# Performance work log

Hardware: AMD Instinct MI355X
Metric: run time of the kernel (lower is better)

Reference implementation:

```python
import jax, jax.numpy as jnp
import numpy as np

K = 7          # kernel_size
PAD = 3        # (K + (K-1)*(dilation-1) - 1)//2 with dilation=1
G = 16         # groups = channels // group_channels = 256 // 16
GC = 16        # group_channels (hardcoded in module)
BN_EPS = 1e-5


def setup_inputs() -> dict:
    key = jax.random.key(0)
    ks = jax.random.split(key, 6)
    C = 256
    Cr = C // 4           # 64
    O2 = K * K * G        # 784
    x = jax.random.normal(ks[0], (4, C, 56, 56), dtype=jnp.float32)
    w1 = jax.random.normal(ks[1], (Cr, C), dtype=jnp.float32) * (1.0 / np.sqrt(C))
    bn_gamma = jnp.ones((Cr,), dtype=jnp.float32)
    bn_beta = jnp.zeros((Cr,), dtype=jnp.float32)
    bn_mean = jax.random.normal(ks[2], (Cr,), dtype=jnp.float32) * 0.1
    bn_var = jax.random.uniform(ks[3], (Cr,), dtype=jnp.float32, minval=0.5, maxval=1.5)
    w2 = jax.random.normal(ks[4], (O2, Cr), dtype=jnp.float32) * (1.0 / np.sqrt(Cr))
    b2 = jnp.zeros((O2,), dtype=jnp.float32)
    return {"x": x, "w1": w1, "bn_gamma": bn_gamma, "bn_beta": bn_beta,
            "bn_mean": bn_mean, "bn_var": bn_var, "w2": w2, "b2": b2}


def reference(x, w1, bn_gamma, bn_beta, bn_mean, bn_var, w2, b2):
    b, C, H, W = x.shape
    # --- weight branch: conv1 (1x1) + BN(eval) + ReLU, then conv2 (1x1) ---
    y = jnp.einsum('oc,bchw->bohw', w1, x)
    scale = bn_gamma * jax.lax.rsqrt(bn_var + BN_EPS)
    y = jax.nn.relu(y * scale[None, :, None, None]
                    + (bn_beta - bn_mean * scale)[None, :, None, None])
    w = jnp.einsum('oc,bchw->bohw', w2, y) + b2[None, :, None, None]
    w = w.reshape(b, G, K * K, H, W)                       # per-pixel dynamic kernels
    # --- unfold: overlapping KxK patches (stride=1, dilation=1, pad=3) ---
    xp = jnp.pad(x, ((0, 0), (0, 0), (PAD, PAD), (PAD, PAD)))
    patches = jnp.stack([xp[:, :, i:i + H, j:j + W]
                         for i in range(K) for j in range(K)], axis=2)  # [b,C,K2,H,W]
    patches = patches.reshape(b, G, GC, K * K, H, W)
    # --- dynamic multiply-reduce over kernel positions ---
    out = jnp.einsum('bgkhw,bgckhw->bgchw', w, patches)
    return out.reshape(b, C, H, W)
```

## Files before the change

kernel.cpp:

```cpp
#include <hip/hip_runtime.h>


#define HW    3136
#define WIDE  56
#define C_IN  256
#define CR    64
#define GC    16
#define KK    49
#define BN_EPS 1e-5f

typedef __attribute__((ext_vector_type(8))) short short8;
typedef __attribute__((ext_vector_type(4))) float f32x4;
typedef __attribute__((ext_vector_type(2))) unsigned int u32x2;

__device__ __forceinline__ unsigned short f2bf(float f) {
    unsigned u = __float_as_uint(f);
    return (unsigned short)((u + 0x7FFFu + ((u >> 16) & 1u)) >> 16);
}

__global__ __launch_bounds__(256) void prep_kernel(
    const float* __restrict__ w1, const float* __restrict__ w2,
    const float* __restrict__ b2,
    unsigned short* __restrict__ w1bf, unsigned short* __restrict__ wprep,
    float* __restrict__ b2pad)
{
    const int t = blockIdx.x * 256 + threadIdx.x;
    if (t < 16384) {
        w1bf[t] = f2bf(w1[t]);
    }
    {
        const int g = t >> 12, k = (t >> 6) & 63, c = t & 63;
        wprep[t] = (k < KK) ? f2bf(w2[(size_t)(g * KK + k) * CR + c]) : (unsigned short)0;
    }
    if (t < 1024) {
        const int g = t >> 6, k = t & 63;
        b2pad[t] = (k < KK) ? b2[g * KK + k] : 0.f;
    }
}

__device__ __forceinline__ int xs_byte(int px, int c) {
    return ((px << 9) + (c << 1)) ^ ((px & 7) << 4);
}

__global__ __launch_bounds__(256) void conv1_bn_relu(
    const float* __restrict__ x, const unsigned short* __restrict__ w1bf,
    const float* __restrict__ gamma, const float* __restrict__ beta,
    const float* __restrict__ mean, const float* __restrict__ var,
    unsigned short* __restrict__ ybf)
{
    __shared__ unsigned short xs[64 * 256];

    const int t    = threadIdx.x;
    const int lane = t & 63;
    const int q    = __builtin_amdgcn_readfirstlane(t >> 6);
    const int tile = blockIdx.x;
    const int b    = tile / 49;
    const int hw0  = (tile - b * 49) * 64;

    {
        const int px = lane;
        const int cb = q * 64;
        const float* __restrict__ xb = x + ((size_t)b * C_IN + cb) * HW + hw0 + px;
#pragma unroll
        for (int i = 0; i < 8; ++i) {
            short8 pk;
#pragma unroll
            for (int j = 0; j < 8; ++j)
                pk[j] = (short)f2bf(xb[(size_t)(i * 8 + j) * HW]);
            *(short8*)((char*)xs + xs_byte(px, cb + i * 8)) = pk;
        }
    }
    __syncthreads();

    const int l15 = lane & 15;
    const int lg  = lane >> 4;
    const int px  = q * 16 + l15;

    f32x4 acc[4];
#pragma unroll
    for (int mt = 0; mt < 4; ++mt) acc[mt] = (f32x4){0.f, 0.f, 0.f, 0.f};

#pragma unroll
    for (int kk = 0; kk < 8; ++kk) {
        const short8 Bf = *(const short8*)((const char*)xs + xs_byte(px, kk * 32 + lg * 8));
#pragma unroll
        for (int mt = 0; mt < 4; ++mt) {
            const short8 Af = *(const short8*)(w1bf + (mt * 16 + l15) * C_IN + kk * 32 + lg * 8);
            acc[mt] = __builtin_amdgcn_mfma_f32_16x16x32_bf16(Af, Bf, acc[mt], 0, 0, 0);
        }
    }

#pragma unroll
    for (int mt = 0; mt < 4; ++mt) {
        const int o0 = mt * 16 + lg * 4;
        const f32x4 ga = *(const f32x4*)(gamma + o0);
        const f32x4 be = *(const f32x4*)(beta + o0);
        const f32x4 mn = *(const f32x4*)(mean + o0);
        const f32x4 va = *(const f32x4*)(var + o0);
        unsigned short o4[4];
#pragma unroll
        for (int r = 0; r < 4; ++r) {
            const float sc = ga[r] * rsqrtf(va[r] + BN_EPS);
            const float sh = be[r] - mn[r] * sc;
            o4[r] = f2bf(fmaxf(acc[mt][r] * sc + sh, 0.f));
        }
        u32x2 pk;
        pk.x = (unsigned)o4[0] | ((unsigned)o4[1] << 16);
        pk.y = (unsigned)o4[2] | ((unsigned)o4[3] << 16);
        *(u32x2*)(ybf + ((size_t)(b * HW + hw0 + px)) * 64 + o0) = pk;
    }
}

__global__ __launch_bounds__(64) void conv2_involution(
    const float* __restrict__ x, const unsigned short* __restrict__ ybf,
    const unsigned short* __restrict__ wprep, const float* __restrict__ b2pad,
    float* __restrict__ out)
{
    __shared__ float kw_lds[64 * 64];

    const int tid  = threadIdx.x;
    const int l15  = tid & 15;
    const int lg   = tid >> 4;
    const int tile = blockIdx.x;
    const int g    = blockIdx.y & 15;
    const int b    = blockIdx.y >> 4;

    {
        short8 Bf[4][2], Af[4][2];
#pragma unroll
        for (int ct = 0; ct < 4; ++ct) {
            const int hwp = tile * 64 + ct * 16 + l15;
            const unsigned short* yb = ybf + ((size_t)(b * HW + hwp)) * 64 + lg * 8;
            Bf[ct][0] = *(const short8*)(yb);
            Bf[ct][1] = *(const short8*)(yb + 32);
        }
#pragma unroll
        for (int rt = 0; rt < 4; ++rt) {
            const unsigned short* ar = wprep + g * 4096 + (rt * 16 + l15) * 64 + lg * 8;
            Af[rt][0] = *(const short8*)(ar);
            Af[rt][1] = *(const short8*)(ar + 32);
        }
        f32x4 acc[4][4];
#pragma unroll
        for (int ct = 0; ct < 4; ++ct)
#pragma unroll
            for (int rt = 0; rt < 4; ++rt) {
                acc[ct][rt] = (f32x4){0.f, 0.f, 0.f, 0.f};
                acc[ct][rt] = __builtin_amdgcn_mfma_f32_16x16x32_bf16(Af[rt][0], Bf[ct][0], acc[ct][rt], 0, 0, 0);
                acc[ct][rt] = __builtin_amdgcn_mfma_f32_16x16x32_bf16(Af[rt][1], Bf[ct][1], acc[ct][rt], 0, 0, 0);
            }

        float bias[4][4];
#pragma unroll
        for (int rt = 0; rt < 4; ++rt)
#pragma unroll
            for (int r = 0; r < 4; ++r)
                bias[rt][r] = b2pad[g * 64 + rt * 16 + lg * 4 + r];

#pragma unroll
        for (int ct = 0; ct < 4; ++ct) {
            const int pxc = ct * 16 + l15;
            const int hwp = tile * 64 + pxc;
            const int hp  = hwp / WIDE;
            const int wp  = hwp - hp * WIDE;
#pragma unroll
            for (int rt = 0; rt < 4; ++rt)
#pragma unroll
                for (int r = 0; r < 4; ++r) {
                    const int k  = rt * 16 + lg * 4 + r;
                    const int i7 = k / 7, j7 = k - i7 * 7;
                    const int rr = hp + i7 - 3, cc = wp + j7 - 3;
                    const bool valid = (k < KK) & (rr >= 0) & (rr < WIDE) &
                                       (cc >= 0) & (cc < WIDE);
                    kw_lds[k * 64 + pxc] = valid ? (acc[ct][rt][r] + bias[rt][r]) : 0.f;
                }
        }
    }
    __syncthreads();

    const int pg   = tid & 15;
    const int cq   = tid >> 4;
    const int hw4  = tile * 64 + pg * 4;
    const int hrow = hw4 / WIDE;
    const int hcol = hw4 - hrow * WIDE;

    const float* bp[4];
#pragma unroll
    for (int c = 0; c < 4; ++c)
        bp[c] = x + ((size_t)b * C_IN + g * GC + cq * 4 + c) * HW;

    float acc2[4][4];
#pragma unroll
    for (int c = 0; c < 4; ++c)
#pragma unroll
        for (int p = 0; p < 4; ++p) acc2[c][p] = 0.f;

#pragma unroll
    for (int i = 0; i < 7; ++i) {
        const int rc    = min(max(hrow + i - 3, 0), WIDE - 1);
        const int basef = rc * WIDE + hcol;
        const int i0 = max(basef - 4, 0);
        const int i2 = min(basef + 4, HW - 4);

        float win[4][12];
#pragma unroll
        for (int c = 0; c < 4; ++c) {
            const f32x4 A0 = *(const f32x4*)(bp[c] + i0);
            const f32x4 A1 = *(const f32x4*)(bp[c] + basef);
            const f32x4 A2 = *(const f32x4*)(bp[c] + i2);
#pragma unroll
            for (int e = 0; e < 4; ++e) {
                win[c][e]     = A0[e];
                win[c][e + 4] = A1[e];
                win[c][e + 8] = A2[e];
            }
        }
#pragma unroll
        for (int jj = 0; jj < 7; ++jj) {
            const f32x4 kw4 = *(const f32x4*)&kw_lds[(i * 7 + jj) * 64 + pg * 4];
#pragma unroll
            for (int c = 0; c < 4; ++c)
#pragma unroll
                for (int p = 0; p < 4; ++p)
                    acc2[c][p] += kw4[p] * win[c][p + jj + 1];
        }
    }

#pragma unroll
    for (int c = 0; c < 4; ++c) {
        f32x4 st;
#pragma unroll
        for (int p = 0; p < 4; ++p) st[p] = acc2[c][p];
        *(f32x4*)(out + ((size_t)b * C_IN + g * GC + cq * 4 + c) * HW + hw4) = st;
    }
}

extern "C" void kernel_launch(void* const* d_in, const int* in_sizes, int n_in,
                              void* d_out, int out_size, void* d_ws, size_t ws_size,
                              hipStream_t stream) {
    const float* x     = (const float*)d_in[0];
    const float* w1    = (const float*)d_in[1];
    const float* gamma = (const float*)d_in[2];
    const float* beta  = (const float*)d_in[3];
    const float* mean  = (const float*)d_in[4];
    const float* var   = (const float*)d_in[5];
    const float* w2    = (const float*)d_in[6];
    const float* b2    = (const float*)d_in[7];
    float* out = (float*)d_out;

    char* ws = (char*)d_ws;
    unsigned short* ybf   = (unsigned short*)(ws);
    unsigned short* wprep = (unsigned short*)(ws + 1605632);
    float*          b2pad = (float*)(ws + 1736704);
    unsigned short* w1bf  = (unsigned short*)(ws + 1740800);

    prep_kernel<<<dim3(256), dim3(256), 0, stream>>>(w1, w2, b2, w1bf, wprep, b2pad);
    conv1_bn_relu<<<dim3(196), dim3(256), 0, stream>>>(x, w1bf, gamma, beta, mean, var, ybf);
    conv2_involution<<<dim3(49, 64), dim3(64), 0, stream>>>(x, ybf, wprep, b2pad, out);
}
```

Baseline: 40.85 us.

## Stage input halo rows in LDS and double threads per involution block

The involution kernel now cooperatively loads a 9-row halo of the 16 group channels into shared memory, with zero-padded column borders. The 7x7 window is then read from LDS instead of from global memory with clamped indices. The block grows to 128 threads (two waves), and each thread now handles 2 channels instead of 4. The MFMA weight generation is split across the two waves, each doing two column tiles. This cuts redundant global loads and raises parallelism, at the cost of more LDS use (about 51KB) and possible bank conflicts, which may limit occupancy.

```diff
diff --git a/kernel.cpp b/kernel.cpp
--- a/kernel.cpp
+++ b/kernel.cpp
@@ -111,69 +111,86 @@
     }
 }
 
-__global__ __launch_bounds__(64) void conv2_involution(
+__global__ __launch_bounds__(128) void conv2_involution(
     const float* __restrict__ x, const unsigned short* __restrict__ ybf,
     const unsigned short* __restrict__ wprep, const float* __restrict__ b2pad,
     float* __restrict__ out)
 {
-    __shared__ float kw_lds[64 * 64];
+    __shared__ float xs[16 * 612];
+    __shared__ float kw_lds[KK * 64];
 
     const int tid  = threadIdx.x;
-    const int l15  = tid & 15;
-    const int lg   = tid >> 4;
     const int tile = blockIdx.x;
     const int g    = blockIdx.y & 15;
     const int b    = blockIdx.y >> 4;
-
-    {
-        short8 Bf[4][2], Af[4][2];
-#pragma unroll
-        for (int ct = 0; ct < 4; ++ct) {
-            const int hwp = tile * 64 + ct * 16 + l15;
+    const int r0   = (tile * 64) / WIDE;
+    const int base_row = r0 - 3;
+
+    {
+        const float* __restrict__ xg = x + ((size_t)b * C_IN + g * GC) * HW;
+#pragma unroll
+        for (int it = 0; it < 16; ++it) {
+            const int id = it * 128 + tid;
+            if (id < 2016) {
+                const int c   = id / 126;
+                const int rem = id - c * 126;
+                const int j   = rem / 14;
+                const int c4  = rem - j * 14;
+                const int gr  = min(max(base_row + j, 0), WIDE - 1);
+                const f32x4 v = *(const f32x4*)(xg + (size_t)c * HW + gr * WIDE + c4 * 4);
+                *(f32x4*)&xs[c * 612 + j * 68 + 4 + c4 * 4] = v;
+            }
+        }
+#pragma unroll
+        for (int it = 0; it < 3; ++it) {
+            const int p = it * 128 + tid;
+            if (p < 288) {
+                const int c    = p / 18;
+                const int rem  = p - c * 18;
+                const int j    = rem >> 1;
+                const int side = rem & 1;
+                *(f32x4*)&xs[c * 612 + j * 68 + (side ? 60 : 0)] = (f32x4){0.f, 0.f, 0.f, 0.f};
+            }
+        }
+    }
+
+    {
+        const int lane = tid & 63;
+        const int wv   = __builtin_amdgcn_readfirstlane(tid >> 6);
+        const int l15  = lane & 15;
+        const int lg   = lane >> 4;
+#pragma unroll
+        for (int cti = 0; cti < 2; ++cti) {
+            const int ct  = wv + cti * 2;
+            const int px  = ct * 16 + l15;
+            const int hwp = tile * 64 + px;
             const unsigned short* yb = ybf + ((size_t)(b * HW + hwp)) * 64 + lg * 8;
-            Bf[ct][0] = *(const short8*)(yb);
-            Bf[ct][1] = *(const short8*)(yb + 32);
-        }
-#pragma unroll
-        for (int rt = 0; rt < 4; ++rt) {
-            const unsigned short* ar = wprep + g * 4096 + (rt * 16 + l15) * 64 + lg * 8;
-            Af[rt][0] = *(const short8*)(ar);
-            Af[rt][1] = *(const short8*)(ar + 32);
-        }
-        f32x4 acc[4][4];
-#pragma unroll
-        for (int ct = 0; ct < 4; ++ct)
+            const short8 B0 = *(const short8*)(yb);
+            const short8 B1 = *(const short8*)(yb + 32);
+            const int hp = hwp / WIDE;
+            const int wp = hwp - hp * WIDE;
+
 #pragma unroll
             for (int rt = 0; rt < 4; ++rt) {
-                acc[ct][rt] = (f32x4){0.f, 0.f, 0.f, 0.f};
-                acc[ct][rt] = __builtin_amdgcn_mfma_f32_16x16x32_bf16(Af[rt][0], Bf[ct][0], acc[ct][rt], 0, 0, 0);
-                acc[ct][rt] = __builtin_amdgcn_mfma_f32_16x16x32_bf16(Af[rt][1], Bf[ct][1], acc[ct][rt], 0, 0, 0);
-            }
-
-        float bias[4][4];
-#pragma unroll
-        for (int rt = 0; rt < 4; ++rt)
-#pragma unroll
-            for (int r = 0; r < 4; ++r)
-                bias[rt][r] = b2pad[g * 64 + rt * 16 + lg * 4 + r];
-
-#pragma unroll
-        for (int ct = 0; ct < 4; ++ct) {
-            const int pxc = ct * 16 + l15;
-            const int hwp = tile * 64 + pxc;
-            const int hp  = hwp / WIDE;
-            const int wp  = hwp - hp * WIDE;
-#pragma unroll
-            for (int rt = 0; rt < 4; ++rt)
+                const unsigned short* ar = wprep + g * 4096 + (rt * 16 + l15) * 64 + lg * 8;
+                const short8 A0 = *(const short8*)(ar);
+                const short8 A1 = *(const short8*)(ar + 32);
+                f32x4 acc = (f32x4){0.f, 0.f, 0.f, 0.f};
+                acc = __builtin_amdgcn_mfma_f32_16x16x32_bf16(A0, B0, acc, 0, 0, 0);
+                acc = __builtin_amdgcn_mfma_f32_16x16x32_bf16(A1, B1, acc, 0, 0, 0);
 #pragma unroll
                 for (int r = 0; r < 4; ++r) {
-                    const int k  = rt * 16 + lg * 4 + r;
-                    const int i7 = k / 7, j7 = k - i7 * 7;
-                    const int rr = hp + i7 - 3, cc = wp + j7 - 3;
-                    const bool valid = (k < KK) & (rr >= 0) & (rr < WIDE) &
-                                       (cc >= 0) & (cc < WIDE);
-                    kw_lds[k * 64 + pxc] = valid ? (acc[ct][rt][r] + bias[rt][r]) : 0.f;
+                    const int k = rt * 16 + lg * 4 + r;
+                    if (k < KK) {
+                        const float val = acc[r] + b2pad[g * 64 + k];
+                        const int i7 = k / 7, j7 = k - i7 * 7;
+                        const int rr = hp + i7 - 3, cc = wp + j7 - 3;
+                        const bool valid = (rr >= 0) & (rr < WIDE) &
+                                           (cc >= 0) & (cc < WIDE);
+                        kw_lds[k * 64 + px] = valid ? val : 0.f;
+                    }
                 }
+            }
         }
     }
     __syncthreads();
@@ -183,56 +200,56 @@
     const int hw4  = tile * 64 + pg * 4;
     const int hrow = hw4 / WIDE;
     const int hcol = hw4 - hrow * WIDE;
-
-    const float* bp[4];
-#pragma unroll
-    for (int c = 0; c < 4; ++c)
-        bp[c] = x + ((size_t)b * C_IN + g * GC + cq * 4 + c) * HW;
-
-    float acc2[4][4];
-#pragma unroll
-    for (int c = 0; c < 4; ++c)
+    const int srow = hrow - r0;
+
+    const int xb0 = (cq * 2) * 612 + srow * 68 + hcol;
+
+    float acc2[2][4];
+#pragma unroll
+    for (int c = 0; c < 2; ++c)
 #pragma unroll
         for (int p = 0; p < 4; ++p) acc2[c][p] = 0.f;
 
 #pragma unroll
     for (int i = 0; i < 7; ++i) {
-        const int rc    = min(max(hrow + i - 3, 0), WIDE - 1);
-        const int basef = rc * WIDE + hcol;
-        const int i0 = max(basef - 4, 0);
-        const int i2 = min(basef + 4, HW - 4);
-
-        float win[4][12];
-#pragma unroll
-        for (int c = 0; c < 4; ++c) {
-            const f32x4 A0 = *(const f32x4*)(bp[c] + i0);
-            const f32x4 A1 = *(const f32x4*)(bp[c] + basef);
-            const f32x4 A2 = *(const f32x4*)(bp[c] + i2);
+        const int rb0 = xb0 + i * 68;
+        const int rb1 = rb0 + 612;
+
+        float win[2][12];
+        {
+            const f32x4 A0 = *(const f32x4*)&xs[rb0];
+            const f32x4 A1 = *(const f32x4*)&xs[rb0 + 4];
+            const f32x4 A2 = *(const f32x4*)&xs[rb0 + 8];
+            const f32x4 B0 = *(const f32x4*)&xs[rb1];
+            const f32x4 B1 = *(const f32x4*)&xs[rb1 + 4];
+            const f32x4 B2 = *(const f32x4*)&xs[rb1 + 8];
 #pragma unroll
             for (int e = 0; e < 4; ++e) {
-                win[c][e]     = A0[e];
-                win[c][e + 4] = A1[e];
-                win[c][e + 8] = A2[e];
+                win[0][e]     = A0[e];
+                win[0][e + 4] = A1[e];
+                win[0][e + 8] = A2[e];
+                win[1][e]     = B0[e];
+                win[1][e + 4] = B1[e];
+                win[1][e + 8] = B2[e];
             }
         }
 #pragma unroll
         for (int jj = 0; jj < 7; ++jj) {
             const f32x4 kw4 = *(const f32x4*)&kw_lds[(i * 7 + jj) * 64 + pg * 4];
 #pragma unroll
-            for (int c = 0; c < 4; ++c)
+            for (int c = 0; c < 2; ++c)
 #pragma unroll
                 for (int p = 0; p < 4; ++p)
                     acc2[c][p] += kw4[p] * win[c][p + jj + 1];
         }
     }
 
-#pragma unroll
-    for (int c = 0; c < 4; ++c) {
-        f32x4 st;
-#pragma unroll
-        for (int p = 0; p < 4; ++p) st[p] = acc2[c][p];
-        *(f32x4*)(out + ((size_t)b * C_IN + g * GC + cq * 4 + c) * HW + hw4) = st;
-    }
+    f32x4 st0, st1;
+#pragma unroll
+    for (int p = 0; p < 4; ++p) { st0[p] = acc2[0][p]; st1[p] = acc2[1][p]; }
+    float* __restrict__ ob = out + ((size_t)b * C_IN + g * GC + cq * 2) * HW + hw4;
+    *(f32x4*)(ob)      = st0;
+    *(f32x4*)(ob + HW) = st1;
 }
 
 extern "C" void kernel_launch(void* const* d_in, const int* in_sizes, int n_in,
@@ -256,5 +273,5 @@
 
     prep_kernel<<<dim3(256), dim3(256), 0, stream>>>(w1, w2, b2, w1bf, wprep, b2pad);
     conv1_bn_relu<<<dim3(196), dim3(256), 0, stream>>>(x, w1bf, gamma, beta, mean, var, ybf);
-    conv2_involution<<<dim3(49, 64), dim3(64), 0, stream>>>(x, ybf, wprep, b2pad, out);
-}
+    conv2_involution<<<dim3(49, 64), dim3(128), 0, stream>>>(x, ybf, wprep, b2pad, out);
+}
```

Measured after the change: 64.03 us. 56.8% more time.

## Stage x as zero-padded bf16 planes for involution window loads

Applied to the files above, without the earlier changes.

Adds a pre-pass kernel that converts x to bf16 and stores each channel plane with a 3-pixel zero border (62x64 rows). The involution stage then reads its 7x7 windows from this padded bf16 buffer, which removes the per-row clamp and index arithmetic and halves the bytes fetched per window. The cost is an extra kernel launch and an extra full pass over x, and rounding the patch values to bf16 loses some precision compared with the fp32 reads.

```diff
diff --git a/kernel.cpp b/kernel.cpp
--- a/kernel.cpp
+++ b/kernel.cpp
@@ -8,14 +8,21 @@
 #define GC    16
 #define KK    49
 #define BN_EPS 1e-5f
+#define PROW  62
+#define PCOL  64
+#define PSTR  (PROW * PCOL)
 
 typedef __attribute__((ext_vector_type(8))) short short8;
+typedef __attribute__((ext_vector_type(4))) short s16x4;
 typedef __attribute__((ext_vector_type(4))) float f32x4;
 typedef __attribute__((ext_vector_type(2))) unsigned int u32x2;
 
 __device__ __forceinline__ unsigned short f2bf(float f) {
     unsigned u = __float_as_uint(f);
     return (unsigned short)((u + 0x7FFFu + ((u >> 16) & 1u)) >> 16);
+}
+__device__ __forceinline__ float bf2f(unsigned short v) {
+    return __uint_as_float(((unsigned)v) << 16);
 }
 
 __global__ __launch_bounds__(256) void prep_kernel(
@@ -36,6 +43,37 @@
         const int g = t >> 6, k = t & 63;
         b2pad[t] = (k < KK) ? b2[g * KK + k] : 0.f;
     }
+}
+
+__global__ __launch_bounds__(256) void xpad_kernel(
+    const float* __restrict__ x, unsigned short* __restrict__ xbf)
+{
+    const int id = blockIdx.x * 256 + threadIdx.x;
+    if (id >= 1024 * PROW) return;
+    const int plane = id / PROW;
+    const int prow  = id - plane * PROW;
+    const int gr    = prow - 3;
+
+    unsigned short row[PCOL];
+    if (gr >= 0 && gr < WIDE) {
+        const float* __restrict__ src = x + (size_t)plane * HW + gr * WIDE;
+#pragma unroll
+        for (int e = 0; e < 4; ++e) { row[e] = 0; row[60 + e] = 0; }
+#pragma unroll
+        for (int v = 0; v < 14; ++v) {
+            const f32x4 a = *(const f32x4*)(src + v * 4);
+#pragma unroll
+            for (int e = 0; e < 4; ++e) row[4 + v * 4 + e] = f2bf(a[e]);
+        }
+    } else {
+#pragma unroll
+        for (int e = 0; e < PCOL; ++e) row[e] = 0;
+    }
+
+    unsigned short* __restrict__ dst = xbf + (size_t)plane * PSTR + prow * PCOL;
+#pragma unroll
+    for (int v = 0; v < 8; ++v)
+        *(short8*)(dst + v * 8) = *(short8*)&row[v * 8];
 }
 
 __device__ __forceinline__ int xs_byte(int px, int c) {
@@ -114,7 +152,7 @@
 __global__ __launch_bounds__(64) void conv2_involution(
     const float* __restrict__ x, const unsigned short* __restrict__ ybf,
     const unsigned short* __restrict__ wprep, const float* __restrict__ b2pad,
-    float* __restrict__ out)
+    const unsigned short* __restrict__ xbf, float* __restrict__ out)
 {
     __shared__ float kw_lds[64 * 64];
 
@@ -184,10 +222,12 @@
     const int hrow = hw4 / WIDE;
     const int hcol = hw4 - hrow * WIDE;
 
-    const float* bp[4];
+    const int e0 = hrow * PCOL + hcol;
+    const int pl0 = b * C_IN + g * GC + cq * 4;
+    const char* pb[4];
 #pragma unroll
     for (int c = 0; c < 4; ++c)
-        bp[c] = x + ((size_t)b * C_IN + g * GC + cq * 4 + c) * HW;
+        pb[c] = (const char*)(xbf + (size_t)(pl0 + c) * PSTR + e0);
 
     float acc2[4][4];
 #pragma unroll
@@ -197,22 +237,17 @@
 
 #pragma unroll
     for (int i = 0; i < 7; ++i) {
-        const int rc    = min(max(hrow + i - 3, 0), WIDE - 1);
-        const int basef = rc * WIDE + hcol;
-        const int i0 = max(basef - 4, 0);
-        const int i2 = min(basef + 4, HW - 4);
-
         float win[4][12];
 #pragma unroll
         for (int c = 0; c < 4; ++c) {
-            const f32x4 A0 = *(const f32x4*)(bp[c] + i0);
-            const f32x4 A1 = *(const f32x4*)(bp[c] + basef);
-            const f32x4 A2 = *(const f32x4*)(bp[c] + i2);
+            const s16x4 s0 = *(const s16x4*)(pb[c] + i * 128 + 0);
+            const s16x4 s1 = *(const s16x4*)(pb[c] + i * 128 + 8);
+            const s16x4 s2 = *(const s16x4*)(pb[c] + i * 128 + 16);
 #pragma unroll
             for (int e = 0; e < 4; ++e) {
-                win[c][e]     = A0[e];
-                win[c][e + 4] = A1[e];
-                win[c][e + 8] = A2[e];
+                win[c][e]     = bf2f((unsigned short)s0[e]);
+                win[c][e + 4] = bf2f((unsigned short)s1[e]);
+                win[c][e + 8] = bf2f((unsigned short)s2[e]);
             }
         }
 #pragma unroll
@@ -231,7 +266,7 @@
         f32x4 st;
 #pragma unroll
         for (int p = 0; p < 4; ++p) st[p] = acc2[c][p];
-        *(f32x4*)(out + ((size_t)b * C_IN + g * GC + cq * 4 + c) * HW + hw4) = st;
+        *(f32x4*)(out + ((size_t)(pl0 + c)) * HW + hw4) = st;
     }
 }
 
@@ -253,8 +288,10 @@
     unsigned short* wprep = (unsigned short*)(ws + 1605632);
     float*          b2pad = (float*)(ws + 1736704);
     unsigned short* w1bf  = (unsigned short*)(ws + 1740800);
+    unsigned short* xbf   = (unsigned short*)(ws + 1773568);
 
     prep_kernel<<<dim3(256), dim3(256), 0, stream>>>(w1, w2, b2, w1bf, wprep, b2pad);
+    xpad_kernel<<<dim3(248), dim3(256), 0, stream>>>(x, xbf);
     conv1_bn_relu<<<dim3(196), dim3(256), 0, stream>>>(x, w1bf, gamma, beta, mean, var, ybf);
-    conv2_involution<<<dim3(49, 64), dim3(64), 0, stream>>>(x, ybf, wprep, b2pad, out);
-}
+    conv2_involution<<<dim3(49, 64), dim3(64), 0, stream>>>(x, ybf, wprep, b2pad, xbf, out);
+}
```

Result: slower. 47.48 us (+16.2%).

## Split involution work across four waves per block with LDS partial-sum reduction

Applied to the files above, without the earlier changes.

The conv2_involution kernel grows from one wave to four waves per block. The MFMA kernel-weight generation is split by pixel column tile across waves, and the 7 kernel rows of the multiply-reduce are split across waves (2,2,2,1). The x window loads for both rows are issued up front, and partial accumulators are reduced through shared memory before the store. This raises parallelism and latency hiding per block, at the cost of an extra barrier, more LDS traffic and an uneven row split between waves.

```diff
diff --git a/kernel.cpp b/kernel.cpp
--- a/kernel.cpp
+++ b/kernel.cpp
@@ -111,127 +111,144 @@
     }
 }
 
-__global__ __launch_bounds__(64) void conv2_involution(
+__global__ __launch_bounds__(256) void conv2_involution(
     const float* __restrict__ x, const unsigned short* __restrict__ ybf,
     const unsigned short* __restrict__ wprep, const float* __restrict__ b2pad,
     float* __restrict__ out)
 {
-    __shared__ float kw_lds[64 * 64];
+    __shared__ float kw_lds[KK * 64];
+    __shared__ float pacc[4 * 64 * 20];
 
     const int tid  = threadIdx.x;
-    const int l15  = tid & 15;
-    const int lg   = tid >> 4;
+    const int lane = tid & 63;
+    const int w    = __builtin_amdgcn_readfirstlane(tid >> 6);
+    const int l15  = lane & 15;
+    const int lg   = lane >> 4;
     const int tile = blockIdx.x;
     const int g    = blockIdx.y & 15;
     const int b    = blockIdx.y >> 4;
 
     {
-        short8 Bf[4][2], Af[4][2];
-#pragma unroll
-        for (int ct = 0; ct < 4; ++ct) {
-            const int hwp = tile * 64 + ct * 16 + l15;
-            const unsigned short* yb = ybf + ((size_t)(b * HW + hwp)) * 64 + lg * 8;
-            Bf[ct][0] = *(const short8*)(yb);
-            Bf[ct][1] = *(const short8*)(yb + 32);
-        }
+        const int px  = w * 16 + l15;
+        const int hwp = tile * 64 + px;
+        const unsigned short* yb = ybf + ((size_t)(b * HW + hwp)) * 64 + lg * 8;
+        const short8 B0 = *(const short8*)(yb);
+        const short8 B1 = *(const short8*)(yb + 32);
+        const int hp = hwp / WIDE;
+        const int wp = hwp - hp * WIDE;
+
 #pragma unroll
         for (int rt = 0; rt < 4; ++rt) {
             const unsigned short* ar = wprep + g * 4096 + (rt * 16 + l15) * 64 + lg * 8;
-            Af[rt][0] = *(const short8*)(ar);
-            Af[rt][1] = *(const short8*)(ar + 32);
-        }
-        f32x4 acc[4][4];
-#pragma unroll
-        for (int ct = 0; ct < 4; ++ct)
-#pragma unroll
-            for (int rt = 0; rt < 4; ++rt) {
-                acc[ct][rt] = (f32x4){0.f, 0.f, 0.f, 0.f};
-                acc[ct][rt] = __builtin_amdgcn_mfma_f32_16x16x32_bf16(Af[rt][0], Bf[ct][0], acc[ct][rt], 0, 0, 0);
-                acc[ct][rt] = __builtin_amdgcn_mfma_f32_16x16x32_bf16(Af[rt][1], Bf[ct][1], acc[ct][rt], 0, 0, 0);
-            }
-
-        float bias[4][4];
-#pragma unroll
-        for (int rt = 0; rt < 4; ++rt)
-#pragma unroll
-            for (int r = 0; r < 4; ++r)
-                bias[rt][r] = b2pad[g * 64 + rt * 16 + lg * 4 + r];
-
-#pragma unroll
-        for (int ct = 0; ct < 4; ++ct) {
-            const int pxc = ct * 16 + l15;
-            const int hwp = tile * 64 + pxc;
-            const int hp  = hwp / WIDE;
-            const int wp  = hwp - hp * WIDE;
-#pragma unroll
-            for (int rt = 0; rt < 4; ++rt)
-#pragma unroll
-                for (int r = 0; r < 4; ++r) {
-                    const int k  = rt * 16 + lg * 4 + r;
+            const short8 A0 = *(const short8*)(ar);
+            const short8 A1 = *(const short8*)(ar + 32);
+            f32x4 acc = (f32x4){0.f, 0.f, 0.f, 0.f};
+            acc = __builtin_amdgcn_mfma_f32_16x16x32_bf16(A0, B0, acc, 0, 0, 0);
+            acc = __builtin_amdgcn_mfma_f32_16x16x32_bf16(A1, B1, acc, 0, 0, 0);
+#pragma unroll
+            for (int r = 0; r < 4; ++r) {
+                const int k = rt * 16 + lg * 4 + r;
+                if (k < KK) {
+                    const float val = acc[r] + b2pad[g * 64 + k];
                     const int i7 = k / 7, j7 = k - i7 * 7;
                     const int rr = hp + i7 - 3, cc = wp + j7 - 3;
-                    const bool valid = (k < KK) & (rr >= 0) & (rr < WIDE) &
+                    const bool valid = (rr >= 0) & (rr < WIDE) &
                                        (cc >= 0) & (cc < WIDE);
-                    kw_lds[k * 64 + pxc] = valid ? (acc[ct][rt][r] + bias[rt][r]) : 0.f;
+                    kw_lds[k * 64 + px] = valid ? val : 0.f;
                 }
+            }
         }
     }
     __syncthreads();
 
-    const int pg   = tid & 15;
-    const int cq   = tid >> 4;
-    const int hw4  = tile * 64 + pg * 4;
-    const int hrow = hw4 / WIDE;
-    const int hcol = hw4 - hrow * WIDE;
-
-    const float* bp[4];
-#pragma unroll
-    for (int c = 0; c < 4; ++c)
-        bp[c] = x + ((size_t)b * C_IN + g * GC + cq * 4 + c) * HW;
-
-    float acc2[4][4];
-#pragma unroll
-    for (int c = 0; c < 4; ++c)
-#pragma unroll
-        for (int p = 0; p < 4; ++p) acc2[c][p] = 0.f;
-
-#pragma unroll
-    for (int i = 0; i < 7; ++i) {
-        const int rc    = min(max(hrow + i - 3, 0), WIDE - 1);
-        const int basef = rc * WIDE + hcol;
-        const int i0 = max(basef - 4, 0);
-        const int i2 = min(basef + 4, HW - 4);
-
-        float win[4][12];
+    {
+        const int pg   = lane & 15;
+        const int cq   = lane >> 4;
+        const int hw4  = tile * 64 + pg * 4;
+        const int hrow = hw4 / WIDE;
+        const int hcol = hw4 - hrow * WIDE;
+
+        const float* bp[4];
+#pragma unroll
+        for (int c = 0; c < 4; ++c)
+            bp[c] = x + ((size_t)b * C_IN + g * GC + cq * 4 + c) * HW;
+
+        const int nr  = (w == 3) ? 1 : 2;
+        const int i0r = 2 * w;
+
+        f32x4 W[2][4][3];
+#pragma unroll
+        for (int ri = 0; ri < 2; ++ri) {
+            if (ri < nr) {
+                const int i     = i0r + ri;
+                const int rc    = min(max(hrow + i - 3, 0), WIDE - 1);
+                const int basef = rc * WIDE + hcol;
+                const int i0 = max(basef - 4, 0);
+                const int i2 = min(basef + 4, HW - 4);
+#pragma unroll
+                for (int c = 0; c < 4; ++c) {
+                    W[ri][c][0] = *(const f32x4*)(bp[c] + i0);
+                    W[ri][c][1] = *(const f32x4*)(bp[c] + basef);
+                    W[ri][c][2] = *(const f32x4*)(bp[c] + i2);
+                }
+            }
+        }
+
+        float acc2[4][4];
+#pragma unroll
+        for (int c = 0; c < 4; ++c)
+#pragma unroll
+            for (int p = 0; p < 4; ++p) acc2[c][p] = 0.f;
+
+#pragma unroll
+        for (int ri = 0; ri < 2; ++ri) {
+            if (ri < nr) {
+                const int i = i0r + ri;
+                float win[4][12];
+#pragma unroll
+                for (int c = 0; c < 4; ++c)
+#pragma unroll
+                    for (int e = 0; e < 4; ++e) {
+                        win[c][e]     = W[ri][c][0][e];
+                        win[c][e + 4] = W[ri][c][1][e];
+                        win[c][e + 8] = W[ri][c][2][e];
+                    }
+#pragma unroll
+                for (int jj = 0; jj < 7; ++jj) {
+                    const f32x4 kw4 = *(const f32x4*)&kw_lds[(i * 7 + jj) * 64 + pg * 4];
+#pragma unroll
+                    for (int c = 0; c < 4; ++c)
+#pragma unroll
+                        for (int p = 0; p < 4; ++p)
+                            acc2[c][p] += kw4[p] * win[c][p + jj + 1];
+                }
+            }
+        }
+
 #pragma unroll
         for (int c = 0; c < 4; ++c) {
-            const f32x4 A0 = *(const f32x4*)(bp[c] + i0);
-            const f32x4 A1 = *(const f32x4*)(bp[c] + basef);
-            const f32x4 A2 = *(const f32x4*)(bp[c] + i2);
-#pragma unroll
-            for (int e = 0; e < 4; ++e) {
-                win[c][e]     = A0[e];
-                win[c][e + 4] = A1[e];
-                win[c][e + 8] = A2[e];
-            }
-        }
-#pragma unroll
-        for (int jj = 0; jj < 7; ++jj) {
-            const f32x4 kw4 = *(const f32x4*)&kw_lds[(i * 7 + jj) * 64 + pg * 4];
-#pragma unroll
-            for (int c = 0; c < 4; ++c)
-#pragma unroll
-                for (int p = 0; p < 4; ++p)
-                    acc2[c][p] += kw4[p] * win[c][p + jj + 1];
-        }
-    }
-
-#pragma unroll
-    for (int c = 0; c < 4; ++c) {
-        f32x4 st;
-#pragma unroll
-        for (int p = 0; p < 4; ++p) st[p] = acc2[c][p];
-        *(f32x4*)(out + ((size_t)b * C_IN + g * GC + cq * 4 + c) * HW + hw4) = st;
+            f32x4 st;
+#pragma unroll
+            for (int p = 0; p < 4; ++p) st[p] = acc2[c][p];
+            *(f32x4*)&pacc[w * 1280 + lane * 20 + c * 4] = st;
+        }
+    }
+    __syncthreads();
+
+    {
+        const int t = tid & 63;
+        const int c = tid >> 6;
+        const int base = t * 20 + c * 4;
+        const f32x4 s0 = *(const f32x4*)&pacc[base];
+        const f32x4 s1 = *(const f32x4*)&pacc[1280 + base];
+        const f32x4 s2 = *(const f32x4*)&pacc[2560 + base];
+        const f32x4 s3 = *(const f32x4*)&pacc[3840 + base];
+        const f32x4 sum = s0 + s1 + s2 + s3;
+
+        const int pg = t & 15;
+        const int cq = t >> 4;
+        const int hw4 = tile * 64 + pg * 4;
+        *(f32x4*)(out + ((size_t)b * C_IN + g * GC + cq * 4 + c) * HW + hw4) = sum;
     }
 }
 
@@ -256,5 +273,5 @@
 
     prep_kernel<<<dim3(256), dim3(256), 0, stream>>>(w1, w2, b2, w1bf, wprep, b2pad);
     conv1_bn_relu<<<dim3(196), dim3(256), 0, stream>>>(x, w1bf, gamma, beta, mean, var, ybf);
-    conv2_involution<<<dim3(49, 64), dim3(64), 0, stream>>>(x, ybf, wprep, b2pad, out);
-}
+    conv2_involution<<<dim3(49, 64), dim3(256), 0, stream>>>(x, ybf, wprep, b2pad, out);
+}
```

Result: slower. 46.22 us (+13.2%).
